# Kernel optimization log

Hardware: AMD Instinct MI355X
Metric: run time of the kernel (lower is better)

Reference implementation:

```python
import jax, jax.numpy as jnp
import numpy as np

S, B, H = 2048, 2, 2048
NP = 16            # num attention heads
HN = H // NP       # head dim = 128


def setup_inputs() -> dict:
    key = jax.random.key(0)
    k0, k1, k2 = jax.random.split(key, 3)
    hidden_states = jax.random.normal(k0, (S, B, H), dtype=jnp.float32) * 0.02
    w_qkv = jax.random.normal(k1, (3 * H, H), dtype=jnp.float32) * 0.02
    b_qkv = jnp.zeros((3 * H,), dtype=jnp.float32)
    w_dense = jax.random.normal(k2, (H, H), dtype=jnp.float32) * 0.02
    b_dense = jnp.zeros((H,), dtype=jnp.float32)
    # causal mask: True means "mask out" (strictly upper triangular)
    attention_mask = jnp.triu(jnp.ones((S, S), dtype=bool), k=1)[None, None]  # [1,1,S,S]
    return {
        "hidden_states": hidden_states,
        "attention_mask": attention_mask,
        "w_qkv": w_qkv,
        "b_qkv": b_qkv,
        "w_dense": w_dense,
        "b_dense": b_dense,
    }


def reference(hidden_states, attention_mask, w_qkv, b_qkv, w_dense, b_dense):
    s, b, h = hidden_states.shape
    # fused QKV projection (ColumnParallelLinear: y = x @ W^T + b)
    mixed = hidden_states @ w_qkv.T + b_qkv                 # [s,b,3h]
    mixed = mixed.reshape(s, b, NP, 3 * HN)
    q, k, v = jnp.split(mixed, 3, axis=-1)                  # each [s,b,np,hn]
    norm = 1.0 / jnp.sqrt(jnp.asarray(HN, hidden_states.dtype))
    # scaled QK^T -> [b,np,sq,sk]
    scores = jnp.einsum("sbnh,tbnh->bnst", q, k) * norm
    # attention_mask_func: masked_fill(mask, -10000.0)
    scores = jnp.where(attention_mask, jnp.asarray(-10000.0, scores.dtype), scores)
    # softmax in fp32 (softmax_in_fp32)
    probs = jax.nn.softmax(scores.astype(jnp.float32), axis=-1).astype(scores.dtype)
    # AV matmul -> [s,b,np,hn] -> [s,b,h]
    context = jnp.einsum("bnst,tbnh->sbnh", probs, v).reshape(s, b, h)
    # output projection (RowParallelLinear)
    out = context @ w_dense.T + b_dense
    return out
```

## Files before the change

kernel.cpp:

```cpp
#include <hip/hip_runtime.h>
#include <hip/hip_bf16.h>
#include <cstdint>
#include <cstddef>

#define SS   2048
#define BB   2
#define HH   2048
#define NHEAD 16
#define HDIM 128
#define H3   6144
#define MROWS 4096

typedef __attribute__((ext_vector_type(4))) float f32x4;
typedef __attribute__((ext_vector_type(8))) __bf16 bf16x8;
typedef __attribute__((ext_vector_type(8))) unsigned short us8;
typedef __attribute__((ext_vector_type(4))) unsigned short us4;

__device__ __forceinline__ unsigned short f2b_hw(float f) {
    return __builtin_bit_cast(unsigned short, (__bf16)f);
}

__device__ __forceinline__ float exp2_fast(float x) {
    float r;
    asm("v_exp_f32 %0, %1" : "=v"(r) : "v"(x));
    return r;
}

__device__ __forceinline__ bf16x8 ld_b16x8(const unsigned short* p) {
    us8 u = *(const us8*)p;
    return __builtin_bit_cast(bf16x8, u);
}

__device__ __forceinline__ bf16x8 ld8_off(const unsigned short* base, int byteoff) {
    return __builtin_bit_cast(bf16x8, *(const us8*)((const char*)base + byteoff));
}

__device__ __forceinline__ int sw256(int b) { return b ^ (((b >> 8) & 7) << 4); }
__device__ __forceinline__ int sw128(int b) { return b ^ (((b >> 7) & 7) << 4); }

__device__ __forceinline__ void gload_lds16(const unsigned short* g, unsigned short* l) {
    __builtin_amdgcn_global_load_lds(
        (const __attribute__((address_space(1))) unsigned int*)g,
        (__attribute__((address_space(3))) unsigned int*)l, 16, 0, 0);
}

__global__ __launch_bounds__(256) void cvt_f32_bf16(
    const float* __restrict__ in, unsigned short* __restrict__ out, int n4)
{
    const int stride = gridDim.x * blockDim.x;
    for (int i = blockIdx.x * blockDim.x + threadIdx.x; i < n4; i += stride) {
        const float4 v = ((const float4*)in)[i];
        us4 o = { f2b_hw(v.x), f2b_hw(v.y), f2b_hw(v.z), f2b_hw(v.w) };
        ((us4*)out)[i] = o;
    }
}

__global__ __launch_bounds__(256) void transpose_v(
    const unsigned short* __restrict__ mixed,
    unsigned short* __restrict__ vt)
{
    const int st = blockIdx.x;
    const int nh = blockIdx.y;
    const int bb = blockIdx.z;
    const int tid = threadIdx.x;
    __shared__ unsigned short T[64][136];
#pragma unroll
    for (int i = 0; i < 4; ++i) {
        const int c = i * 256 + tid;
        const int sl = c >> 4, d0 = (c & 15) << 3;
        const us8 v = *(const us8*)(mixed +
            ((size_t)(st * 64 + sl) * BB + bb) * H3 + nh * 384 + 256 + d0);
        *(us8*)(&T[sl][d0]) = v;
    }
    __syncthreads();
#pragma unroll
    for (int i = 0; i < 4; ++i) {
        const int c = i * 256 + tid;
        const int d = c >> 3, sl0 = (c & 7) << 3;
        us8 o;
#pragma unroll
        for (int j = 0; j < 8; ++j) o[j] = T[sl0 + j][d];
        *(us8*)(vt + ((size_t)(bb * NHEAD + nh) * HDIM + d) * SS + st * 64 + sl0) = o;
    }
}

#define STAGE_UNIT(gp, lo)                                        \
    gload_lds16((gp) + soff[0], smem + (lo) + tid * 8);           \
    gload_lds16((gp) + soff[1], smem + (lo) + 4096 + tid * 8);

template <int BN, bool F32OUT>
__global__ __launch_bounds__(512, 2) void gemm_8ph(
    const unsigned short* __restrict__ A,
    const unsigned short* __restrict__ Bw,
    const float* __restrict__ bias,
    void* __restrict__ Cout,
    int Nv, int Kv)
{
    extern __shared__ unsigned short smem[];
    constexpr int NF     = BN / 64;
    constexpr int BUNITS = BN / 128;
    constexpr int BELEMS = BN * 64;

    const int tid  = threadIdx.x;
    const int lane = tid & 63;
    const int wave = tid >> 6;
    const int wm = wave >> 2, wn = wave & 3;
    const int bm = blockIdx.y, bn = blockIdx.x;

    const unsigned short* Ab = A  + (size_t)bm * 128 * Kv;
    const unsigned short* Bb = Bw + (size_t)bn * BN * Kv;

    int soff[2];
#pragma unroll
    for (int i = 0; i < 2; ++i) {
        const int p = (i * 512 + tid) * 16;
        const int l = p ^ (((p >> 7) & 7) << 4);
        soff[i] = (l >> 7) * Kv + ((l & 127) >> 1);
    }

    f32x4 acc[4][NF];
#pragma unroll
    for (int m = 0; m < 4; ++m)
#pragma unroll
        for (int n = 0; n < NF; ++n) acc[m][n] = (f32x4){0.f, 0.f, 0.f, 0.f};

    const int frow = lane & 15;
    const int g16  = (lane >> 4) << 4;
    const int swx  = (frow & 7) << 4;
    const int kx0  = g16 ^ swx;
    const int kx1  = (64 + g16) ^ swx;
    const int aRow = (wm * 64 + frow) * 128;
    const int bRow = 32768 + (wn * (BN / 4) + frow) * 128;

    const int NT = Kv >> 6;

    STAGE_UNIT(Ab, 0);
    STAGE_UNIT(Bb, 16384);
    STAGE_UNIT(Bb + 128 * Kv, 16384 + 8192);
    if constexpr (BUNITS == 3) { STAGE_UNIT(Bb + 256 * Kv, 16384 + 16384); }
    STAGE_UNIT(Bb + 64, 16384 + BELEMS);
    STAGE_UNIT(Bb + 128 * Kv + 64, 16384 + BELEMS + 8192);
    if constexpr (BUNITS == 3) { STAGE_UNIT(Bb + 256 * Kv + 64, 16384 + BELEMS + 16384); }
    if constexpr (BUNITS == 3) { asm volatile("s_waitcnt vmcnt(6)" ::: "memory"); }
    else                       { asm volatile("s_waitcnt vmcnt(4)" ::: "memory"); }
    __builtin_amdgcn_s_barrier();

    for (int t = 0; t < NT; ++t) {
        const int j  = t & 1;
        const int jn = j ^ 1;
        const int aj = j * 16384;
        const int bj = j * (BN * 128);
        const int cA = ((t + 1 < NT) ? (t + 1) : (NT - 1)) * 64;
        const int cB = ((t + 2 < NT) ? (t + 2) : (NT - 1)) * 64;

        bf16x8 bbf[NF][2];

        {
            bf16x8 a00 = ld8_off(smem, aj + aRow + 0 * 2048 + kx0);
            bf16x8 a01 = ld8_off(smem, aj + aRow + 0 * 2048 + kx1);
            bf16x8 a10 = ld8_off(smem, aj + aRow + 1 * 2048 + kx0);
            bf16x8 a11 = ld8_off(smem, aj + aRow + 1 * 2048 + kx1);
#pragma unroll
            for (int n = 0; n < NF; ++n) {
                bbf[n][0] = ld8_off(smem, bj + bRow + n * 2048 + kx0);
                bbf[n][1] = ld8_off(smem, bj + bRow + n * 2048 + kx1);
            }
            STAGE_UNIT(Ab + cA, jn * 8192);
            __builtin_amdgcn_s_barrier();
            __builtin_amdgcn_s_setprio(1);
#pragma unroll
            for (int n = 0; n < NF; ++n) {
                acc[0][n] = __builtin_amdgcn_mfma_f32_16x16x32_bf16(a00, bbf[n][0], acc[0][n], 0, 0, 0);
                acc[0][n] = __builtin_amdgcn_mfma_f32_16x16x32_bf16(a01, bbf[n][1], acc[0][n], 0, 0, 0);
                acc[1][n] = __builtin_amdgcn_mfma_f32_16x16x32_bf16(a10, bbf[n][0], acc[1][n], 0, 0, 0);
                acc[1][n] = __builtin_amdgcn_mfma_f32_16x16x32_bf16(a11, bbf[n][1], acc[1][n], 0, 0, 0);
            }
            __builtin_amdgcn_s_setprio(0);
        }
        {
            bf16x8 a00 = ld8_off(smem, aj + aRow + 2 * 2048 + kx0);
            bf16x8 a01 = ld8_off(smem, aj + aRow + 2 * 2048 + kx1);
            bf16x8 a10 = ld8_off(smem, aj + aRow + 3 * 2048 + kx0);
            bf16x8 a11 = ld8_off(smem, aj + aRow + 3 * 2048 + kx1);
            STAGE_UNIT(Bb + cB, 16384 + j * BELEMS);
            STAGE_UNIT(Bb + 128 * Kv + cB, 16384 + j * BELEMS + 8192);
            if constexpr (BUNITS == 3) {
                STAGE_UNIT(Bb + 256 * Kv + cB, 16384 + j * BELEMS + 16384);
            }
            __builtin_amdgcn_s_barrier();
            __builtin_amdgcn_s_setprio(1);
#pragma unroll
            for (int n = 0; n < NF; ++n) {
                acc[2][n] = __builtin_amdgcn_mfma_f32_16x16x32_bf16(a00, bbf[n][0], acc[2][n], 0, 0, 0);
                acc[2][n] = __builtin_amdgcn_mfma_f32_16x16x32_bf16(a01, bbf[n][1], acc[2][n], 0, 0, 0);
                acc[3][n] = __builtin_amdgcn_mfma_f32_16x16x32_bf16(a10, bbf[n][0], acc[3][n], 0, 0, 0);
                acc[3][n] = __builtin_amdgcn_mfma_f32_16x16x32_bf16(a11, bbf[n][1], acc[3][n], 0, 0, 0);
            }
            __builtin_amdgcn_s_setprio(0);
            if constexpr (BUNITS == 3) { asm volatile("s_waitcnt vmcnt(6)" ::: "memory"); }
            else                       { asm volatile("s_waitcnt vmcnt(4)" ::: "memory"); }
        }
    }

    const int r0 = (lane >> 4) << 2;
#pragma unroll
    for (int m = 0; m < 4; ++m) {
        const int row = bm * 128 + wm * 64 + m * 16 + r0;
#pragma unroll
        for (int n = 0; n < NF; ++n) {
            const int col = bn * BN + wn * (BN / 4) + n * 16 + frow;
            const float bv = bias[col];
            float scale = 1.0f;
            if constexpr (!F32OUT) {
                if ((col % 384) < 128)
                    scale = (float)(0.08838834764831843 * 1.4426950408889634);
            }
#pragma unroll
            for (int r = 0; r < 4; ++r) {
                const float o = (acc[m][n][r] + bv) * scale;
                if (F32OUT) ((float*)Cout)[(size_t)(row + r) * Nv + col] = o;
                else        ((unsigned short*)Cout)[(size_t)(row + r) * Nv + col] = f2b_hw(o);
            }
        }
    }
}

__global__ __launch_bounds__(256) void attn_kernel(
    const unsigned short* __restrict__ mixed,
    const unsigned short* __restrict__ vt,
    unsigned short* __restrict__ context)
{
    const int id   = blockIdx.x;
    const int c    = id & 7;
    const int k    = id >> 3;
    const int pair = k & 15;
    const int nhbb = c + 8 * (k >> 4);
    const int nh   = nhbb >> 1;
    const int bb   = nhbb & 1;

    const int tid  = threadIdx.x;
    const int lane = tid & 63;
    const int wave = tid >> 6;

    __shared__ __align__(1024) unsigned short smem[16384 + 16384 + 4096];

    const int frow = lane & 15;
    const int g16  = (lane >> 4) << 4;
    const int r0   = (lane >> 4) << 2;

    int koff[4], voff[4];
#pragma unroll
    for (int i = 0; i < 4; ++i) {
        const int p0 = (i * 256 + tid) * 16;
        const int lK = p0 ^ (((p0 >> 8) & 7) << 4);
        koff[i] = (lK >> 8) * (BB * H3) + ((lK & 255) >> 1);
        const int lV = p0 ^ (((p0 >> 7) & 7) << 4);
        voff[i] = (lV >> 7) * SS + ((lV & 127) >> 1);
    }

    const unsigned short* kg = mixed + (size_t)bb * H3 + nh * 384 + 128;
    const unsigned short* vg = vt + (size_t)(bb * NHEAD + nh) * HDIM * SS;

    char* Pb = (char*)(smem + 32768) + wave * 2048;

    bf16x8 ones;
#pragma unroll
    for (int j = 0; j < 8; ++j) ones[j] = (__bf16)1.0f;

    for (int half = 0; half < 2; ++half) {
        const int qt = half ? (31 - pair) : pair;
        const int q0 = qt * 64 + wave * 16;

        bf16x8 qf[4];
        {
            const unsigned short* qptr =
                mixed + ((size_t)(q0 + frow) * BB + bb) * H3 + nh * 384;
#pragma unroll
            for (int kk = 0; kk < 4; ++kk)
                qf[kk] = ld_b16x8(qptr + kk * 32 + ((lane >> 4) << 3));
        }

        f32x4 Oacc[8];
#pragma unroll
        for (int ct = 0; ct < 8; ++ct) Oacc[ct] = (f32x4){0.f, 0.f, 0.f, 0.f};
        f32x4 lacc = (f32x4){0.f, 0.f, 0.f, 0.f};
        float m_r[4] = {-1e30f, -1e30f, -1e30f, -1e30f};

        {
            unsigned short* Kd = smem + wave * 512;
            unsigned short* Vd = smem + 16384 + wave * 512;
#pragma unroll
            for (int i = 0; i < 4; ++i) {
                gload_lds16(kg + koff[i], Kd + i * 2048);
                gload_lds16(vg + voff[i], Vd + i * 2048);
            }
        }
        __syncthreads();

        int cur = 0;
        for (int kt = 0; kt <= qt; ++kt) {
            if (kt < qt) {
                const unsigned short* kt_g = kg + (size_t)(kt + 1) * 64 * (BB * H3);
                const unsigned short* vt_g = vg + (kt + 1) * 64;
                unsigned short* Kd = smem + (cur ^ 1) * 8192 + wave * 512;
                unsigned short* Vd = smem + 16384 + (cur ^ 1) * 8192 + wave * 512;
#pragma unroll
                for (int i = 0; i < 4; ++i) {
                    gload_lds16(kt_g + koff[i], Kd + i * 2048);
                    gload_lds16(vt_g + voff[i], Vd + i * 2048);
                }
            }

            const unsigned short* Ks = smem + cur * 8192;
            const unsigned short* Vs = smem + 16384 + cur * 8192;

            f32x4 sc4[4];
#pragma unroll
            for (int t = 0; t < 4; ++t) {
                f32x4 s = (f32x4){0.f, 0.f, 0.f, 0.f};
#pragma unroll
                for (int kk = 0; kk < 4; ++kk) {
                    bf16x8 kf = ld8_off(Ks, sw256((t * 16 + frow) * 256 + kk * 64 + g16));
                    s = __builtin_amdgcn_mfma_f32_16x16x32_bf16(qf[kk], kf, s, 0, 0, 0);
                }
                sc4[t] = s;
            }

            if (kt == qt) {
#pragma unroll
                for (int t = 0; t < 4; ++t) {
                    const int kcol = qt * 64 + t * 16 + frow;
#pragma unroll
                    for (int r = 0; r < 4; ++r)
                        if (kcol > q0 + r0 + r) sc4[t][r] = -1e30f;
                }
            }

            float pmax[4];
#pragma unroll
            for (int r = 0; r < 4; ++r)
                pmax[r] = fmaxf(fmaxf(sc4[0][r], sc4[1][r]), fmaxf(sc4[2][r], sc4[3][r]));
            bool need = false;
#pragma unroll
            for (int r = 0; r < 4; ++r) need = need || (pmax[r] > m_r[r] + 11.5f);
            if (__any(need)) {
                float tmax[4];
#pragma unroll
                for (int r = 0; r < 4; ++r) {
                    tmax[r] = pmax[r];
                    tmax[r] = fmaxf(tmax[r], __shfl_xor(tmax[r], 1, 64));
                    tmax[r] = fmaxf(tmax[r], __shfl_xor(tmax[r], 2, 64));
                    tmax[r] = fmaxf(tmax[r], __shfl_xor(tmax[r], 4, 64));
                    tmax[r] = fmaxf(tmax[r], __shfl_xor(tmax[r], 8, 64));
                }
                float a_r[4];
#pragma unroll
                for (int r = 0; r < 4; ++r) {
                    const float mnew = fmaxf(m_r[r], tmax[r]);
                    a_r[r] = exp2_fast(m_r[r] - mnew);
                    m_r[r] = mnew;
                    lacc[r] *= a_r[r];
                }
#pragma unroll
                for (int ct = 0; ct < 8; ++ct)
#pragma unroll
                    for (int r = 0; r < 4; ++r) Oacc[ct][r] *= a_r[r];
            }

#pragma unroll
            for (int t = 0; t < 4; ++t)
#pragma unroll
                for (int r = 0; r < 4; ++r)
                    *(unsigned short*)(Pb + sw128((r0 + r) * 128 + (t * 16 + frow) * 2)) =
                        f2b_hw(exp2_fast(sc4[t][r] - m_r[r]));

#pragma unroll
            for (int ks = 0; ks < 2; ++ks) {
                bf16x8 pf = ld8_off((const unsigned short*)Pb, sw128(frow * 128 + ks * 64 + g16));
                lacc = __builtin_amdgcn_mfma_f32_16x16x32_bf16(pf, ones, lacc, 0, 0, 0);
#pragma unroll
                for (int ct = 0; ct < 8; ++ct) {
                    bf16x8 vf = ld8_off(Vs, sw128((ct * 16 + frow) * 128 + ks * 64 + g16));
                    Oacc[ct] = __builtin_amdgcn_mfma_f32_16x16x32_bf16(pf, vf, Oacc[ct], 0, 0, 0);
                }
            }

            __syncthreads();
            cur ^= 1;
        }

        float rl[4];
#pragma unroll
        for (int r = 0; r < 4; ++r) rl[r] = __builtin_amdgcn_rcpf(lacc[r]);
#pragma unroll
        for (int ct = 0; ct < 8; ++ct) {
            const int d = ct * 16 + frow;
#pragma unroll
            for (int r = 0; r < 4; ++r) {
                const size_t row = (size_t)(q0 + r0 + r) * BB + bb;
                context[row * HH + nh * 128 + d] = f2b_hw(Oacc[ct][r] * rl[r]);
            }
        }
    }
}

extern "C" void kernel_launch(void* const* d_in, const int* in_sizes, int n_in,
                              void* d_out, int out_size, void* d_ws, size_t ws_size,
                              hipStream_t stream) {
    const float* hidden  = (const float*)d_in[0];
    const float* w_qkv   = (const float*)d_in[2];
    const float* b_qkv   = (const float*)d_in[3];
    const float* w_dense = (const float*)d_in[4];
    const float* b_dense = (const float*)d_in[5];
    float* out = (float*)d_out;

    unsigned short* mixed = (unsigned short*)d_ws;
    unsigned short* hb    = mixed + (size_t)MROWS * H3;
    unsigned short* wq    = hb + (size_t)MROWS * HH;
    unsigned short* wd    = wq + (size_t)H3 * HH;
    unsigned short* context = hb;
    unsigned short* vtg     = wq;

    dim3 blk(256);
    cvt_f32_bf16<<<2048, blk, 0, stream>>>(hidden, hb, (MROWS * HH) / 4);
    cvt_f32_bf16<<<2048, blk, 0, stream>>>(w_qkv, wq, (H3 * HH) / 4);
    cvt_f32_bf16<<<1024, blk, 0, stream>>>(w_dense, wd, (HH * HH) / 4);

    hipFuncSetAttribute(reinterpret_cast<const void*>(gemm_8ph<384, false>),
                        hipFuncAttributeMaxDynamicSharedMemorySize, 131072);
    gemm_8ph<384, false><<<dim3(H3 / 384, MROWS / 128), dim3(512), 131072, stream>>>(
        hb, wq, b_qkv, mixed, H3, HH);
    transpose_v<<<dim3(32, NHEAD, BB), blk, 0, stream>>>(mixed, vtg);
    attn_kernel<<<dim3(512), blk, 0, stream>>>(mixed, vtg, context);
    hipFuncSetAttribute(reinterpret_cast<const void*>(gemm_8ph<256, true>),
                        hipFuncAttributeMaxDynamicSharedMemorySize, 98304);
    gemm_8ph<256, true><<<dim3(HH / 256, MROWS / 128), dim3(512), 98304, stream>>>(
        context, wd, b_dense, out, HH, HH);
}
```

Before: 237.1 us.

## Use 128-key attention tiles with split K/V single-buffer reload

The attention key tile grows from 64 to 128 keys, which halves the number of loop iterations and barriers per query tile. The K/V double buffer becomes one buffer each for K and V, with the next K loaded right after the QK MFMAs and the next V loaded after the PV MFMAs, so each load overlaps the other half of the work. The P scratch and the V swizzle move to a 256-byte row layout. In exchange the causal diagonal tile wastes more masked work, register pressure rises from the larger score array, and LDS use grows slightly.

```diff
diff --git a/kernel.cpp b/kernel.cpp
--- a/kernel.cpp
+++ b/kernel.cpp
@@ -36,7 +36,6 @@
 }
 
 __device__ __forceinline__ int sw256(int b) { return b ^ (((b >> 8) & 7) << 4); }
-__device__ __forceinline__ int sw128(int b) { return b ^ (((b >> 7) & 7) << 4); }
 
 __device__ __forceinline__ void gload_lds16(const unsigned short* g, unsigned short* l) {
     __builtin_amdgcn_global_load_lds(
@@ -242,26 +241,28 @@
     const int lane = tid & 63;
     const int wave = tid >> 6;
 
-    __shared__ __align__(1024) unsigned short smem[16384 + 16384 + 4096];
+    __shared__ __align__(1024) unsigned short smem[16384 + 16384 + 8192];
 
     const int frow = lane & 15;
     const int g16  = (lane >> 4) << 4;
     const int r0   = (lane >> 4) << 2;
-
-    int koff[4], voff[4];
-#pragma unroll
-    for (int i = 0; i < 4; ++i) {
+    const int kb8  = (lane >> 4) << 3;
+
+    int koff[8], voff[8];
+#pragma unroll
+    for (int i = 0; i < 8; ++i) {
         const int p0 = (i * 256 + tid) * 16;
-        const int lK = p0 ^ (((p0 >> 8) & 7) << 4);
-        koff[i] = (lK >> 8) * (BB * H3) + ((lK & 255) >> 1);
-        const int lV = p0 ^ (((p0 >> 7) & 7) << 4);
-        voff[i] = (lV >> 7) * SS + ((lV & 127) >> 1);
+        const int l  = p0 ^ (((p0 >> 8) & 7) << 4);
+        koff[i] = (l >> 8) * (BB * H3) + ((l & 255) >> 1);
+        voff[i] = (l >> 8) * SS + ((l & 255) >> 1);
     }
 
     const unsigned short* kg = mixed + (size_t)bb * H3 + nh * 384 + 128;
     const unsigned short* vg = vt + (size_t)(bb * NHEAD + nh) * HDIM * SS;
 
-    char* Pb = (char*)(smem + 32768) + wave * 2048;
+    unsigned short* Ksm = smem;
+    unsigned short* Vsm = smem + 16384;
+    char* Pb = (char*)(smem + 32768) + wave * 4096;
 
     bf16x8 ones;
 #pragma unroll
@@ -270,6 +271,7 @@
     for (int half = 0; half < 2; ++half) {
         const int qt = half ? (31 - pair) : pair;
         const int q0 = qt * 64 + wave * 16;
+        const int NT = (qt >> 1) + 1;
 
         bf16x8 qf[4];
         {
@@ -277,7 +279,7 @@
                 mixed + ((size_t)(q0 + frow) * BB + bb) * H3 + nh * 384;
 #pragma unroll
             for (int kk = 0; kk < 4; ++kk)
-                qf[kk] = ld_b16x8(qptr + kk * 32 + ((lane >> 4) << 3));
+                qf[kk] = ld_b16x8(qptr + kk * 32 + kb8);
         }
 
         f32x4 Oacc[8];
@@ -286,50 +288,38 @@
         f32x4 lacc = (f32x4){0.f, 0.f, 0.f, 0.f};
         float m_r[4] = {-1e30f, -1e30f, -1e30f, -1e30f};
 
-        {
-            unsigned short* Kd = smem + wave * 512;
-            unsigned short* Vd = smem + 16384 + wave * 512;
-#pragma unroll
-            for (int i = 0; i < 4; ++i) {
-                gload_lds16(kg + koff[i], Kd + i * 2048);
-                gload_lds16(vg + voff[i], Vd + i * 2048);
-            }
+#pragma unroll
+        for (int i = 0; i < 8; ++i) {
+            gload_lds16(kg + koff[i], Ksm + i * 2048 + tid * 8);
+            gload_lds16(vg + voff[i], Vsm + i * 2048 + tid * 8);
         }
         __syncthreads();
 
-        int cur = 0;
-        for (int kt = 0; kt <= qt; ++kt) {
-            if (kt < qt) {
-                const unsigned short* kt_g = kg + (size_t)(kt + 1) * 64 * (BB * H3);
-                const unsigned short* vt_g = vg + (kt + 1) * 64;
-                unsigned short* Kd = smem + (cur ^ 1) * 8192 + wave * 512;
-                unsigned short* Vd = smem + 16384 + (cur ^ 1) * 8192 + wave * 512;
-#pragma unroll
-                for (int i = 0; i < 4; ++i) {
-                    gload_lds16(kt_g + koff[i], Kd + i * 2048);
-                    gload_lds16(vt_g + voff[i], Vd + i * 2048);
-                }
-            }
-
-            const unsigned short* Ks = smem + cur * 8192;
-            const unsigned short* Vs = smem + 16384 + cur * 8192;
-
-            f32x4 sc4[4];
-#pragma unroll
-            for (int t = 0; t < 4; ++t) {
+        for (int kt = 0; kt < NT; ++kt) {
+            f32x4 sc4[8];
+#pragma unroll
+            for (int t = 0; t < 8; ++t) {
                 f32x4 s = (f32x4){0.f, 0.f, 0.f, 0.f};
 #pragma unroll
                 for (int kk = 0; kk < 4; ++kk) {
-                    bf16x8 kf = ld8_off(Ks, sw256((t * 16 + frow) * 256 + kk * 64 + g16));
+                    bf16x8 kf = ld8_off(Ksm, sw256((t * 16 + frow) * 256 + kk * 64 + g16));
                     s = __builtin_amdgcn_mfma_f32_16x16x32_bf16(qf[kk], kf, s, 0, 0, 0);
                 }
                 sc4[t] = s;
             }
 
-            if (kt == qt) {
-#pragma unroll
-                for (int t = 0; t < 4; ++t) {
-                    const int kcol = qt * 64 + t * 16 + frow;
+            __syncthreads();
+            if (kt + 1 < NT) {
+                const unsigned short* kt_g = kg + (size_t)(kt + 1) * 128 * (BB * H3);
+#pragma unroll
+                for (int i = 0; i < 8; ++i)
+                    gload_lds16(kt_g + koff[i], Ksm + i * 2048 + tid * 8);
+            }
+
+            if (kt == NT - 1) {
+#pragma unroll
+                for (int t = 0; t < 8; ++t) {
+                    const int kcol = (kt << 7) + t * 16 + frow;
 #pragma unroll
                     for (int r = 0; r < 4; ++r)
                         if (kcol > q0 + r0 + r) sc4[t][r] = -1e30f;
@@ -338,8 +328,11 @@
 
             float pmax[4];
 #pragma unroll
-            for (int r = 0; r < 4; ++r)
-                pmax[r] = fmaxf(fmaxf(sc4[0][r], sc4[1][r]), fmaxf(sc4[2][r], sc4[3][r]));
+            for (int r = 0; r < 4; ++r) {
+                float m0 = fmaxf(fmaxf(sc4[0][r], sc4[1][r]), fmaxf(sc4[2][r], sc4[3][r]));
+                float m1 = fmaxf(fmaxf(sc4[4][r], sc4[5][r]), fmaxf(sc4[6][r], sc4[7][r]));
+                pmax[r] = fmaxf(m0, m1);
+            }
             bool need = false;
 #pragma unroll
             for (int r = 0; r < 4; ++r) need = need || (pmax[r] > m_r[r] + 11.5f);
@@ -368,25 +361,30 @@
             }
 
 #pragma unroll
-            for (int t = 0; t < 4; ++t)
+            for (int t = 0; t < 8; ++t)
 #pragma unroll
                 for (int r = 0; r < 4; ++r)
-                    *(unsigned short*)(Pb + sw128((r0 + r) * 128 + (t * 16 + frow) * 2)) =
+                    *(unsigned short*)(Pb + sw256((r0 + r) * 256 + (t * 16 + frow) * 2)) =
                         f2b_hw(exp2_fast(sc4[t][r] - m_r[r]));
 
 #pragma unroll
-            for (int ks = 0; ks < 2; ++ks) {
-                bf16x8 pf = ld8_off((const unsigned short*)Pb, sw128(frow * 128 + ks * 64 + g16));
+            for (int ks = 0; ks < 4; ++ks) {
+                bf16x8 pf = ld8_off((const unsigned short*)Pb, sw256(frow * 256 + ks * 64 + g16));
                 lacc = __builtin_amdgcn_mfma_f32_16x16x32_bf16(pf, ones, lacc, 0, 0, 0);
 #pragma unroll
                 for (int ct = 0; ct < 8; ++ct) {
-                    bf16x8 vf = ld8_off(Vs, sw128((ct * 16 + frow) * 128 + ks * 64 + g16));
+                    bf16x8 vf = ld8_off(Vsm, sw256((ct * 16 + frow) * 256 + ks * 64 + g16));
                     Oacc[ct] = __builtin_amdgcn_mfma_f32_16x16x32_bf16(pf, vf, Oacc[ct], 0, 0, 0);
                 }
             }
 
             __syncthreads();
-            cur ^= 1;
+            if (kt + 1 < NT) {
+                const unsigned short* vt_g = vg + (kt + 1) * 128;
+#pragma unroll
+                for (int i = 0; i < 8; ++i)
+                    gload_lds16(vt_g + voff[i], Vsm + i * 2048 + tid * 8);
+            }
         }
 
         float rl[4];
@@ -401,6 +399,7 @@
                 context[row * HH + nh * 128 + d] = f2b_hw(Oacc[ct][r] * rl[r]);
             }
         }
+        __syncthreads();
     }
 }
 
```

New measurement: 275.8 us. 16.3% more time.

## Replace double-buffered K/V LDS with single buffers and staggered reloads

Applied to the files above, without the earlier changes.

Shrinks the attention kernel's shared memory from double-buffered K and V tiles to single buffers. The next K tile is loaded right after the QK^T step and the next V tile right after the PV step, each behind an added barrier. This cuts LDS use per block, which may let more blocks run per CU. The cost is a second barrier per iteration and less time for each prefetch to land before it is needed.

```diff
diff --git a/kernel.cpp b/kernel.cpp
--- a/kernel.cpp
+++ b/kernel.cpp
@@ -242,11 +242,12 @@
     const int lane = tid & 63;
     const int wave = tid >> 6;
 
-    __shared__ __align__(1024) unsigned short smem[16384 + 16384 + 4096];
+    __shared__ __align__(1024) unsigned short smem[8192 + 8192 + 4096];
 
     const int frow = lane & 15;
     const int g16  = (lane >> 4) << 4;
     const int r0   = (lane >> 4) << 2;
+    const int kb8  = (lane >> 4) << 3;
 
     int koff[4], voff[4];
 #pragma unroll
@@ -261,7 +262,9 @@
     const unsigned short* kg = mixed + (size_t)bb * H3 + nh * 384 + 128;
     const unsigned short* vg = vt + (size_t)(bb * NHEAD + nh) * HDIM * SS;
 
-    char* Pb = (char*)(smem + 32768) + wave * 2048;
+    unsigned short* Ksm = smem;
+    unsigned short* Vsm = smem + 8192;
+    char* Pb = (char*)(smem + 16384) + wave * 2048;
 
     bf16x8 ones;
 #pragma unroll
@@ -277,7 +280,7 @@
                 mixed + ((size_t)(q0 + frow) * BB + bb) * H3 + nh * 384;
 #pragma unroll
             for (int kk = 0; kk < 4; ++kk)
-                qf[kk] = ld_b16x8(qptr + kk * 32 + ((lane >> 4) << 3));
+                qf[kk] = ld_b16x8(qptr + kk * 32 + kb8);
         }
 
         f32x4 Oacc[8];
@@ -286,44 +289,32 @@
         f32x4 lacc = (f32x4){0.f, 0.f, 0.f, 0.f};
         float m_r[4] = {-1e30f, -1e30f, -1e30f, -1e30f};
 
-        {
-            unsigned short* Kd = smem + wave * 512;
-            unsigned short* Vd = smem + 16384 + wave * 512;
-#pragma unroll
-            for (int i = 0; i < 4; ++i) {
-                gload_lds16(kg + koff[i], Kd + i * 2048);
-                gload_lds16(vg + voff[i], Vd + i * 2048);
-            }
+#pragma unroll
+        for (int i = 0; i < 4; ++i) {
+            gload_lds16(kg + koff[i], Ksm + i * 2048 + tid * 8);
+            gload_lds16(vg + voff[i], Vsm + i * 2048 + tid * 8);
         }
         __syncthreads();
 
-        int cur = 0;
         for (int kt = 0; kt <= qt; ++kt) {
-            if (kt < qt) {
-                const unsigned short* kt_g = kg + (size_t)(kt + 1) * 64 * (BB * H3);
-                const unsigned short* vt_g = vg + (kt + 1) * 64;
-                unsigned short* Kd = smem + (cur ^ 1) * 8192 + wave * 512;
-                unsigned short* Vd = smem + 16384 + (cur ^ 1) * 8192 + wave * 512;
-#pragma unroll
-                for (int i = 0; i < 4; ++i) {
-                    gload_lds16(kt_g + koff[i], Kd + i * 2048);
-                    gload_lds16(vt_g + voff[i], Vd + i * 2048);
-                }
-            }
-
-            const unsigned short* Ks = smem + cur * 8192;
-            const unsigned short* Vs = smem + 16384 + cur * 8192;
-
             f32x4 sc4[4];
 #pragma unroll
             for (int t = 0; t < 4; ++t) {
                 f32x4 s = (f32x4){0.f, 0.f, 0.f, 0.f};
 #pragma unroll
                 for (int kk = 0; kk < 4; ++kk) {
-                    bf16x8 kf = ld8_off(Ks, sw256((t * 16 + frow) * 256 + kk * 64 + g16));
+                    bf16x8 kf = ld8_off(Ksm, sw256((t * 16 + frow) * 256 + kk * 64 + g16));
                     s = __builtin_amdgcn_mfma_f32_16x16x32_bf16(qf[kk], kf, s, 0, 0, 0);
                 }
                 sc4[t] = s;
+            }
+
+            __syncthreads();
+            if (kt < qt) {
+                const unsigned short* kt_g = kg + (size_t)(kt + 1) * 64 * (BB * H3);
+#pragma unroll
+                for (int i = 0; i < 4; ++i)
+                    gload_lds16(kt_g + koff[i], Ksm + i * 2048 + tid * 8);
             }
 
             if (kt == qt) {
@@ -380,13 +371,18 @@
                 lacc = __builtin_amdgcn_mfma_f32_16x16x32_bf16(pf, ones, lacc, 0, 0, 0);
 #pragma unroll
                 for (int ct = 0; ct < 8; ++ct) {
-                    bf16x8 vf = ld8_off(Vs, sw128((ct * 16 + frow) * 128 + ks * 64 + g16));
+                    bf16x8 vf = ld8_off(Vsm, sw128((ct * 16 + frow) * 128 + ks * 64 + g16));
                     Oacc[ct] = __builtin_amdgcn_mfma_f32_16x16x32_bf16(pf, vf, Oacc[ct], 0, 0, 0);
                 }
             }
 
             __syncthreads();
-            cur ^= 1;
+            if (kt < qt) {
+                const unsigned short* vt_g = vg + (kt + 1) * 64;
+#pragma unroll
+                for (int i = 0; i < 4; ++i)
+                    gload_lds16(vt_g + voff[i], Vsm + i * 2048 + tid * 8);
+            }
         }
 
         float rl[4];
```

Result: no change. 236.1 us (-0.4%).
